# Kernel tuning notes

Hardware: AMD Instinct MI355X
Metric: run time of the kernel (lower is better)

Reference implementation:

```python
import jax, jax.numpy as jnp
import numpy as np

EPS = 1e-6


def _layernorm(x, g, b):
    mu = jnp.mean(x, axis=-1, keepdims=True)
    var = jnp.mean((x - mu) ** 2, axis=-1, keepdims=True)
    return (x - mu) * jax.lax.rsqrt(var + EPS) * g + b


def _sinusoidal_pe(seq_len, d_model):
    pos = jnp.arange(seq_len, dtype=jnp.float32)[:, None]
    div = jnp.exp(jnp.arange(0, d_model, 2, dtype=jnp.float32) * (-np.log(10000.0) / d_model))
    pe = jnp.zeros((seq_len, d_model), dtype=jnp.float32)
    pe = pe.at[:, 0::2].set(jnp.sin(pos * div))
    pe = pe.at[:, 1::2].set(jnp.cos(pos * div))
    return pe


def setup_inputs() -> dict:
    key = jax.random.key(0)
    ks = jax.random.split(key, 6)
    B, S, D, H = 4, 4096, 1024, 16
    std = 0.02
    return {
        "x": jax.random.normal(ks[0], (B, S, D), jnp.float32),
        "ln1_g": jnp.ones((D,), jnp.float32),
        "ln1_b": jnp.zeros((D,), jnp.float32),
        "w_qkv": jax.random.normal(ks[1], (D, 3 * D), jnp.float32) * std,
        "w_out": jax.random.normal(ks[2], (D, D), jnp.float32) * std,
        "b_out": jnp.zeros((D,), jnp.float32),
        "ln2_g": jnp.ones((D,), jnp.float32),
        "ln2_b": jnp.zeros((D,), jnp.float32),
        "w1": jax.random.normal(ks[3], (D, 2 * D), jnp.float32) * std,
        "b1": jnp.zeros((2 * D,), jnp.float32),
        "w2": jax.random.normal(ks[4], (2 * D, 2 * D), jnp.float32) * std,
        "b2": jnp.zeros((2 * D,), jnp.float32),
        "w3": jax.random.normal(ks[5], (2 * D, D), jnp.float32) * std,
        "b3": jnp.zeros((D,), jnp.float32),
    }


def reference(x, ln1_g, ln1_b, w_qkv, w_out, b_out, ln2_g, ln2_b, w1, b1, w2, b2, w3, b3):
    B, S, D = x.shape
    H = 16
    dh = D // H  # dim_head = 64

    h = _layernorm(x, ln1_g, ln1_b)
    h = h + _sinusoidal_pe(S, D)[None]  # space_dim == 1 -> sinusoidal PE

    # linear (kernelized, non-causal) self-attention: efficient-attention style
    qkv = h @ w_qkv  # [B,S,3D]
    q, k, v = jnp.split(qkv, 3, axis=-1)
    to_heads = lambda t: t.reshape(B, S, H, dh).transpose(0, 2, 1, 3)  # [B,H,S,dh]
    q, k, v = to_heads(q), to_heads(k), to_heads(v)
    q = jax.nn.softmax(q, axis=-1) * (dh ** -0.5)
    k = jax.nn.softmax(k, axis=2)  # softmax over sequence
    context = jnp.einsum('bhnd,bhne->bhde', k, v)  # [B,H,dh,dh]
    attn = jnp.einsum('bhnd,bhde->bhne', q, context)  # [B,H,S,dh]
    attn = attn.transpose(0, 2, 1, 3).reshape(B, S, D)
    attn = attn @ w_out + b_out

    x = x + attn  # residual (dropout p=0)

    y = _layernorm(x, ln2_g, ln2_b)
    y = jax.nn.gelu(y @ w1 + b1, approximate=False)
    y = jax.nn.gelu(y @ w2 + b2, approximate=False)
    y = y @ w3 + b3
    return x + y
```

## Files before the change

kernel.cpp:

```cpp
#include <hip/hip_runtime.h>
#include <cstdint>
#include <cstddef>

#define BB 4
#define SS 4096
#define DD 1024
#define HH 16
#define MM (BB*SS)

typedef __bf16 bf16x8 __attribute__((ext_vector_type(8)));
typedef float  f32x4  __attribute__((ext_vector_type(4)));

__device__ __forceinline__ float b2f(unsigned short h){
    union { unsigned int u; float f; } c; c.u = ((unsigned int)h) << 16; return c.f;
}
__device__ __forceinline__ unsigned short f2b(float f){
    union { float f; unsigned int u; } c; c.f = f;
    unsigned int u = c.u + 0x7FFFu + ((c.u >> 16) & 1u);
    return (unsigned short)(u >> 16);
}

__global__ void transpose_cvt(const float* __restrict__ src, unsigned short* __restrict__ dst,
                              int K, int N){
    __shared__ float tile[32][33];
    int kb = blockIdx.y*32, nb = blockIdx.x*32;
    int tx = threadIdx.x, ty = threadIdx.y;
    for(int i=0;i<32;i+=8) tile[ty+i][tx] = src[(size_t)(kb+ty+i)*N + nb+tx];
    __syncthreads();
    for(int i=0;i<32;i+=8) dst[(size_t)(nb+ty+i)*K + kb+tx] = f2b(tile[tx][ty+i]);
}

__global__ __launch_bounds__(256) void ln_kernel(const float* __restrict__ x,
                                                 const float* __restrict__ g,
                                                 const float* __restrict__ bta,
                                                 unsigned short* __restrict__ out,
                                                 int add_pe){
    int row = blockIdx.x;
    int t = threadIdx.x;
    float4 v = ((const float4*)(x + (size_t)row*DD))[t];
    float s = v.x+v.y+v.z+v.w;
    float q = v.x*v.x+v.y*v.y+v.z*v.z+v.w*v.w;
    for(int off=32; off>0; off>>=1){ s += __shfl_xor(s, off); q += __shfl_xor(q, off); }
    __shared__ float red[8];
    int wv = t>>6, ln = t&63;
    if(ln==0){ red[wv] = s; red[4+wv] = q; }
    __syncthreads();
    s = red[0]+red[1]+red[2]+red[3];
    q = red[4]+red[5]+red[6]+red[7];
    float mu = s * (1.0f/1024.0f);
    float var = q * (1.0f/1024.0f) - mu*mu;
    float rs = rsqrtf(var + 1e-6f);
    int d0 = t*4;
    float4 gg = ((const float4*)g)[t];
    float4 bb = ((const float4*)bta)[t];
    float o0 = (v.x-mu)*rs*gg.x + bb.x;
    float o1 = (v.y-mu)*rs*gg.y + bb.y;
    float o2 = (v.z-mu)*rs*gg.z + bb.z;
    float o3 = (v.w-mu)*rs*gg.w + bb.w;
    if(add_pe){
        int sidx = row & (SS-1);
        const float cfac = -0.008994473019508968f;
        float a0 = (float)sidx * expf(cfac * (float)(d0));
        float a1 = (float)sidx * expf(cfac * (float)(d0 + 2));
        o0 += sinf(a0); o1 += cosf(a0);
        o2 += sinf(a1); o3 += cosf(a1);
    }
    ushort4 o;
    o.x = f2b(o0); o.y = f2b(o1); o.z = f2b(o2); o.w = f2b(o3);
    *(ushort4*)(out + (size_t)row*DD + d0) = o;
}

template<int EPI>
__global__ __launch_bounds__(256, 2) void gemm_bt(
        const unsigned short* __restrict__ A,
        const unsigned short* __restrict__ Bt,
        void* __restrict__ Cout,
        const float* __restrict__ bias,
        const float* __restrict__ resid,
        int M, int N, int K)
{
    __shared__ __align__(16) unsigned short lA[128*64];
    __shared__ __align__(16) unsigned short lB[128*64];
    const int tid  = threadIdx.x;
    const int lane = tid & 63;
    const int wave = tid >> 6;
    const int quad = lane >> 4;
    const int l16  = lane & 15;
    const int wr = wave >> 1, wc = wave & 1;

    int gn  = gridDim.x;
    int lin = blockIdx.y * gn + blockIdx.x;
    int xcd = lin & 7;
    int j   = lin >> 3;
    int mt  = xcd + 8*(j/gn);
    int nt  = j - (j/gn)*gn;
    const int m0 = mt * 128;
    const int n0 = nt * 128;

    f32x4 acc[4][4] = {};

    for (int k0 = 0; k0 < K; k0 += 64) {
        __syncthreads();
        #pragma unroll
        for (int i = 0; i < 4; i++) {
            int c   = tid + 256*i;
            int row = c >> 3;
            int kc  = ((c & 7) ^ (row & 7)) << 3;
            const unsigned short* gA = A  + (size_t)(m0 + row) * K + k0 + kc;
            const unsigned short* gB = Bt + (size_t)(n0 + row) * K + k0 + kc;
            char* lpA = ((char*)lA) + (wave<<10) + (i<<12);
            char* lpB = ((char*)lB) + (wave<<10) + (i<<12);
            __builtin_amdgcn_global_load_lds((const __attribute__((address_space(1))) void*)gA,
                                             (__attribute__((address_space(3))) void*)lpA, 16, 0, 0);
            __builtin_amdgcn_global_load_lds((const __attribute__((address_space(1))) void*)gB,
                                             (__attribute__((address_space(3))) void*)lpB, 16, 0, 0);
        }
        __syncthreads();
        #pragma unroll
        for (int kk = 0; kk < 2; kk++) {
            bf16x8 af[4], bfr[4];
            #pragma unroll
            for (int mi = 0; mi < 4; mi++) {
                int row = wr*64 + mi*16 + l16;
                int kb  = (kk*64 + quad*16) ^ ((row & 7) << 4);
                af[mi] = *(const bf16x8*)((const char*)lA + row*128 + kb);
            }
            #pragma unroll
            for (int ni = 0; ni < 4; ni++) {
                int row = wc*64 + ni*16 + l16;
                int kb  = (kk*64 + quad*16) ^ ((row & 7) << 4);
                bfr[ni] = *(const bf16x8*)((const char*)lB + row*128 + kb);
            }
            #pragma unroll
            for (int mi = 0; mi < 4; mi++)
                #pragma unroll
                for (int ni = 0; ni < 4; ni++)
                    acc[mi][ni] = __builtin_amdgcn_mfma_f32_16x16x32_bf16(af[mi], bfr[ni], acc[mi][ni], 0, 0, 0);
        }
    }

    #pragma unroll
    for (int mi = 0; mi < 4; mi++) {
        #pragma unroll
        for (int r = 0; r < 4; r++) {
            int grow = m0 + wr*64 + mi*16 + quad*4 + r;
            #pragma unroll
            for (int ni = 0; ni < 4; ni++) {
                int gcol = n0 + wc*64 + ni*16 + l16;
                float v = acc[mi][ni][r];
                size_t idx = (size_t)grow * N + gcol;
                if (EPI == 0) {
                    ((unsigned short*)Cout)[idx] = f2b(v);
                } else if (EPI == 1) {
                    v += bias[gcol];
                    v = 0.5f * v * (1.0f + erff(v * 0.70710678118654752f));
                    ((unsigned short*)Cout)[idx] = f2b(v);
                } else {
                    v += bias[gcol] + resid[idx];
                    ((float*)Cout)[idx] = v;
                }
            }
        }
    }
}

__global__ __launch_bounds__(256) void ctx_partial(const unsigned short* __restrict__ qkv,
                                                   float* __restrict__ EP,
                                                   float* __restrict__ CS){
    int sc = blockIdx.x, h = blockIdx.y, b = blockIdx.z;
    int t = threadIdx.x;
    __shared__ __align__(16) float kl[64][64];
    __shared__ __align__(16) float vl[64][64];
    __shared__ float csred[4][64];
    float acc[16] = {};
    float cspart = 0.0f;
    int e = t & 63, dg = (t >> 6) * 16;
    int dcol = t & 63, schunk = t >> 6;
    for(int s0 = 0; s0 < 256; s0 += 64){
        __syncthreads();
        for(int j=0;j<4;j++){
            int lin = t + 256*j;
            int row = lin >> 4;
            int c4  = (lin & 15) * 4;
            size_t gr = (size_t)(b*SS + sc*256 + s0 + row);
            ushort4 kv = *(const ushort4*)(qkv + gr*3072 + DD + h*64 + c4);
            float4 kf; kf.x=expf(b2f(kv.x)); kf.y=expf(b2f(kv.y)); kf.z=expf(b2f(kv.z)); kf.w=expf(b2f(kv.w));
            *(float4*)&kl[row][c4] = kf;
            ushort4 vv = *(const ushort4*)(qkv + gr*3072 + 2*DD + h*64 + c4);
            float4 vf; vf.x=b2f(vv.x); vf.y=b2f(vv.y); vf.z=b2f(vv.z); vf.w=b2f(vv.w);
            *(float4*)&vl[row][c4] = vf;
        }
        __syncthreads();
        #pragma unroll
        for(int i=0;i<16;i++) cspart += kl[schunk*16+i][dcol];
        for(int s=0;s<64;s++){
            float ve = vl[s][e];
            #pragma unroll
            for(int di=0; di<16; di++) acc[di] += kl[s][dg+di] * ve;
        }
    }
    int slot = (b*HH + h)*16 + sc;
    float* ep = EP + (size_t)slot*4096;
    #pragma unroll
    for(int di=0; di<16; di++) ep[(dg+di)*64 + e] = acc[di];
    csred[schunk][dcol] = cspart;
    __syncthreads();
    if(t < 64) CS[slot*64 + t] = csred[0][t]+csred[1][t]+csred[2][t]+csred[3][t];
}

__global__ __launch_bounds__(256) void ctx_reduce(const float* __restrict__ EP,
                                                  const float* __restrict__ CS,
                                                  float* __restrict__ CTXF){
    int bh = blockIdx.x;
    int t = threadIdx.x;
    int d = t >> 2, e0 = (t & 3) * 16;
    float cs = 0.0f;
    #pragma unroll
    for(int sl=0; sl<16; sl++) cs += CS[(bh*16+sl)*64 + d];
    float inv = 1.0f/cs;
    #pragma unroll
    for(int i=0;i<16;i++){
        float s = 0.0f;
        #pragma unroll
        for(int sl=0; sl<16; sl++) s += EP[(size_t)(bh*16+sl)*4096 + d*64 + e0 + i];
        CTXF[(size_t)bh*4096 + d*64 + e0 + i] = s * inv;
    }
}

__global__ __launch_bounds__(256) void attn_heads(const unsigned short* __restrict__ qkv,
                                                  const float* __restrict__ CTXF,
                                                  unsigned short* __restrict__ abuf){
    int rg = blockIdx.x, h = blockIdx.y;
    int b = rg >> 6;
    int t = threadIdx.x;
    __shared__ __align__(16) float cl[64][64];
    __shared__ float ql[64*65];
    const float* cb = CTXF + (size_t)(b*HH + h)*4096;
    for(int j=0;j<4;j++){
        int lin = t + 256*j;
        ((float4*)cl)[lin] = ((const float4*)cb)[lin];
    }
    {
        int r = t >> 2, seg = (t & 3) * 16;
        const unsigned short* qp = qkv + (size_t)(rg*64 + r)*3072 + h*64 + seg;
        float vals[16];
        float m = -1e30f;
        #pragma unroll
        for(int u=0; u<4; u++){
            ushort4 qv = *(const ushort4*)(qp + u*4);
            vals[u*4+0]=b2f(qv.x); vals[u*4+1]=b2f(qv.y); vals[u*4+2]=b2f(qv.z); vals[u*4+3]=b2f(qv.w);
        }
        #pragma unroll
        for(int i=0;i<16;i++) m = fmaxf(m, vals[i]);
        m = fmaxf(m, __shfl_xor(m, 1));
        m = fmaxf(m, __shfl_xor(m, 2));
        float ssum = 0.0f;
        #pragma unroll
        for(int i=0;i<16;i++){ vals[i] = expf(vals[i]-m); ssum += vals[i]; }
        ssum += __shfl_xor(ssum, 1);
        ssum += __shfl_xor(ssum, 2);
        float scl = 0.125f/ssum;
        #pragma unroll
        for(int i=0;i<16;i++) ql[r*65 + seg + i] = vals[i]*scl;
    }
    __syncthreads();
    int e = t & 63, rbase = (t >> 6) * 16;
    float acc2[16] = {};
    for(int d=0; d<64; d++){
        float cv = cl[d][e];
        #pragma unroll
        for(int ri=0; ri<16; ri++) acc2[ri] += ql[(rbase+ri)*65 + d] * cv;
    }
    #pragma unroll
    for(int ri=0; ri<16; ri++)
        abuf[(size_t)(rg*64 + rbase + ri)*DD + h*64 + e] = f2b(acc2[ri]);
}

extern "C" void kernel_launch(void* const* d_in, const int* in_sizes, int n_in,
                              void* d_out, int out_size, void* d_ws, size_t ws_size,
                              hipStream_t stream)
{
    const float* x     = (const float*)d_in[0];
    const float* ln1_g = (const float*)d_in[1];
    const float* ln1_b = (const float*)d_in[2];
    const float* w_qkv = (const float*)d_in[3];
    const float* w_out = (const float*)d_in[4];
    const float* b_out = (const float*)d_in[5];
    const float* ln2_g = (const float*)d_in[6];
    const float* ln2_b = (const float*)d_in[7];
    const float* w1    = (const float*)d_in[8];
    const float* b1    = (const float*)d_in[9];
    const float* w2    = (const float*)d_in[10];
    const float* b2    = (const float*)d_in[11];
    const float* w3    = (const float*)d_in[12];
    const float* b3    = (const float*)d_in[13];

    char* ws = (char*)d_ws;
    unsigned short* wqkvT = (unsigned short*)(ws + 0);
    unsigned short* woutT = (unsigned short*)(ws + 6291456);
    unsigned short* w1T   = (unsigned short*)(ws + 8388608);
    unsigned short* w2T   = (unsigned short*)(ws + 12582912);
    unsigned short* w3T   = (unsigned short*)(ws + 20971520);
    unsigned short* Hbuf  = (unsigned short*)(ws + 25165824);
    unsigned short* QKV   = (unsigned short*)(ws + 58720256);
    float*          EP    = (float*)(ws + 159383552);
    float*          CS    = (float*)(ws + 176160768);
    float*          CTXF  = (float*)(ws + 176422912);
    unsigned short* Abuf  = Hbuf;
    float*          X2    = (float*)(ws + 58720256);
    unsigned short* H2    = Hbuf;
    unsigned short* Y1    = (unsigned short*)d_out;
    unsigned short* Y2    = (unsigned short*)(ws + 125829120);

    dim3 tb(32, 8);
    transpose_cvt<<<dim3(3072/32, 1024/32), tb, 0, stream>>>(w_qkv, wqkvT, 1024, 3072);
    transpose_cvt<<<dim3(1024/32, 1024/32), tb, 0, stream>>>(w_out, woutT, 1024, 1024);
    transpose_cvt<<<dim3(2048/32, 1024/32), tb, 0, stream>>>(w1,    w1T,   1024, 2048);
    transpose_cvt<<<dim3(2048/32, 2048/32), tb, 0, stream>>>(w2,    w2T,   2048, 2048);
    transpose_cvt<<<dim3(1024/32, 2048/32), tb, 0, stream>>>(w3,    w3T,   2048, 1024);

    ln_kernel<<<MM, 256, 0, stream>>>(x, ln1_g, ln1_b, Hbuf, 1);

    gemm_bt<0><<<dim3(3072/128, MM/128), 256, 0, stream>>>(Hbuf, wqkvT, QKV, nullptr, nullptr, MM, 3072, 1024);

    ctx_partial<<<dim3(16, HH, BB), 256, 0, stream>>>(QKV, EP, CS);
    ctx_reduce<<<BB*HH, 256, 0, stream>>>(EP, CS, CTXF);
    attn_heads<<<dim3(256, HH), 256, 0, stream>>>(QKV, CTXF, Abuf);

    gemm_bt<2><<<dim3(1024/128, MM/128), 256, 0, stream>>>(Abuf, woutT, X2, b_out, x, MM, 1024, 1024);

    ln_kernel<<<MM, 256, 0, stream>>>(X2, ln2_g, ln2_b, H2, 0);

    gemm_bt<1><<<dim3(2048/128, MM/128), 256, 0, stream>>>(H2, w1T, Y1, b1, nullptr, MM, 2048, 1024);
    gemm_bt<1><<<dim3(2048/128, MM/128), 256, 0, stream>>>(Y1, w2T, Y2, b2, nullptr, MM, 2048, 2048);
    gemm_bt<2><<<dim3(1024/128, MM/128), 256, 0, stream>>>(Y2, w3T, d_out, b3, X2, MM, 1024, 2048);
}
```

Baseline: 791.7 us.

## Store residual stream in bf16 and register-tile context/attention kernels

The intermediate residual X2 is now written as bf16 instead of fp32, and the second layernorm and final GEMM epilogue read it as bf16. This halves that tensor's write and read traffic but adds rounding error to the residual carried into the output. Separately, ctx_partial and attn_heads switch to 4x4 register tiles with float4 LDS reads, 16-byte global loads and vectorised stores, and a transposed q buffer in LDS, to cut LDS traffic per FMA.

```diff
diff --git a/kernel.cpp b/kernel.cpp
--- a/kernel.cpp
+++ b/kernel.cpp
@@ -13,6 +13,9 @@
 
 __device__ __forceinline__ float b2f(unsigned short h){
     union { unsigned int u; float f; } c; c.u = ((unsigned int)h) << 16; return c.f;
+}
+__device__ __forceinline__ float b2f_u(unsigned int u16){
+    union { unsigned int u; float f; } c; c.u = u16 << 16; return c.f;
 }
 __device__ __forceinline__ unsigned short f2b(float f){
     union { float f; unsigned int u; } c; c.f = f;
@@ -30,14 +33,21 @@
     for(int i=0;i<32;i+=8) dst[(size_t)(nb+ty+i)*K + kb+tx] = f2b(tile[tx][ty+i]);
 }
 
-__global__ __launch_bounds__(256) void ln_kernel(const float* __restrict__ x,
+template<int INBF>
+__global__ __launch_bounds__(256) void ln_kernel(const void* __restrict__ xin,
                                                  const float* __restrict__ g,
                                                  const float* __restrict__ bta,
                                                  unsigned short* __restrict__ out,
                                                  int add_pe){
     int row = blockIdx.x;
     int t = threadIdx.x;
-    float4 v = ((const float4*)(x + (size_t)row*DD))[t];
+    float4 v;
+    if (INBF == 0) {
+        v = ((const float4*)((const float*)xin + (size_t)row*DD))[t];
+    } else {
+        ushort4 u = ((const ushort4*)((const unsigned short*)xin + (size_t)row*DD))[t];
+        v.x = b2f(u.x); v.y = b2f(u.y); v.z = b2f(u.z); v.w = b2f(u.w);
+    }
     float s = v.x+v.y+v.z+v.w;
     float q = v.x*v.x+v.y*v.y+v.z*v.z+v.w*v.w;
     for(int off=32; off>0; off>>=1){ s += __shfl_xor(s, off); q += __shfl_xor(q, off); }
@@ -76,7 +86,7 @@
         const unsigned short* __restrict__ Bt,
         void* __restrict__ Cout,
         const float* __restrict__ bias,
-        const float* __restrict__ resid,
+        const void* __restrict__ resid,
         int M, int N, int K)
 {
     __shared__ __align__(16) unsigned short lA[128*64];
@@ -155,8 +165,11 @@
                     v += bias[gcol];
                     v = 0.5f * v * (1.0f + erff(v * 0.70710678118654752f));
                     ((unsigned short*)Cout)[idx] = f2b(v);
+                } else if (EPI == 2) {
+                    v += bias[gcol] + ((const float*)resid)[idx];
+                    ((unsigned short*)Cout)[idx] = f2b(v);
                 } else {
-                    v += bias[gcol] + resid[idx];
+                    v += bias[gcol] + b2f(((const unsigned short*)resid)[idx]);
                     ((float*)Cout)[idx] = v;
                 }
             }
@@ -172,37 +185,52 @@
     __shared__ __align__(16) float kl[64][64];
     __shared__ __align__(16) float vl[64][64];
     __shared__ float csred[4][64];
-    float acc[16] = {};
+    float acc[4][4] = {};
     float cspart = 0.0f;
-    int e = t & 63, dg = (t >> 6) * 16;
+    int e4 = (t & 15) * 4, d4 = (t >> 4) * 4;
     int dcol = t & 63, schunk = t >> 6;
     for(int s0 = 0; s0 < 256; s0 += 64){
         __syncthreads();
-        for(int j=0;j<4;j++){
+        #pragma unroll
+        for(int j=0;j<2;j++){
             int lin = t + 256*j;
-            int row = lin >> 4;
-            int c4  = (lin & 15) * 4;
+            int row = lin >> 3;
+            int c8  = (lin & 7) * 8;
             size_t gr = (size_t)(b*SS + sc*256 + s0 + row);
-            ushort4 kv = *(const ushort4*)(qkv + gr*3072 + DD + h*64 + c4);
-            float4 kf; kf.x=expf(b2f(kv.x)); kf.y=expf(b2f(kv.y)); kf.z=expf(b2f(kv.z)); kf.w=expf(b2f(kv.w));
-            *(float4*)&kl[row][c4] = kf;
-            ushort4 vv = *(const ushort4*)(qkv + gr*3072 + 2*DD + h*64 + c4);
-            float4 vf; vf.x=b2f(vv.x); vf.y=b2f(vv.y); vf.z=b2f(vv.z); vf.w=b2f(vv.w);
-            *(float4*)&vl[row][c4] = vf;
+            uint4 kv = *(const uint4*)(qkv + gr*3072 + DD + h*64 + c8);
+            float4 ka, kb2;
+            ka.x = expf(b2f_u(kv.x & 0xFFFFu)); ka.y = expf(b2f_u(kv.x >> 16));
+            ka.z = expf(b2f_u(kv.y & 0xFFFFu)); ka.w = expf(b2f_u(kv.y >> 16));
+            kb2.x = expf(b2f_u(kv.z & 0xFFFFu)); kb2.y = expf(b2f_u(kv.z >> 16));
+            kb2.z = expf(b2f_u(kv.w & 0xFFFFu)); kb2.w = expf(b2f_u(kv.w >> 16));
+            *(float4*)&kl[row][c8]   = ka;
+            *(float4*)&kl[row][c8+4] = kb2;
+            uint4 vv = *(const uint4*)(qkv + gr*3072 + 2*DD + h*64 + c8);
+            float4 va, vb;
+            va.x = b2f_u(vv.x & 0xFFFFu); va.y = b2f_u(vv.x >> 16);
+            va.z = b2f_u(vv.y & 0xFFFFu); va.w = b2f_u(vv.y >> 16);
+            vb.x = b2f_u(vv.z & 0xFFFFu); vb.y = b2f_u(vv.z >> 16);
+            vb.z = b2f_u(vv.w & 0xFFFFu); vb.w = b2f_u(vv.w >> 16);
+            *(float4*)&vl[row][c8]   = va;
+            *(float4*)&vl[row][c8+4] = vb;
         }
         __syncthreads();
         #pragma unroll
         for(int i=0;i<16;i++) cspart += kl[schunk*16+i][dcol];
         for(int s=0;s<64;s++){
-            float ve = vl[s][e];
-            #pragma unroll
-            for(int di=0; di<16; di++) acc[di] += kl[s][dg+di] * ve;
+            float4 k4 = *(const float4*)&kl[s][d4];
+            float4 v4 = *(const float4*)&vl[s][e4];
+            acc[0][0] += k4.x*v4.x; acc[0][1] += k4.x*v4.y; acc[0][2] += k4.x*v4.z; acc[0][3] += k4.x*v4.w;
+            acc[1][0] += k4.y*v4.x; acc[1][1] += k4.y*v4.y; acc[1][2] += k4.y*v4.z; acc[1][3] += k4.y*v4.w;
+            acc[2][0] += k4.z*v4.x; acc[2][1] += k4.z*v4.y; acc[2][2] += k4.z*v4.z; acc[2][3] += k4.z*v4.w;
+            acc[3][0] += k4.w*v4.x; acc[3][1] += k4.w*v4.y; acc[3][2] += k4.w*v4.z; acc[3][3] += k4.w*v4.w;
         }
     }
     int slot = (b*HH + h)*16 + sc;
     float* ep = EP + (size_t)slot*4096;
     #pragma unroll
-    for(int di=0; di<16; di++) ep[(dg+di)*64 + e] = acc[di];
+    for(int i=0;i<4;i++)
+        *(float4*)&ep[(d4+i)*64 + e4] = *(float4*)&acc[i][0];
     csred[schunk][dcol] = cspart;
     __syncthreads();
     if(t < 64) CS[slot*64 + t] = csred[0][t]+csred[1][t]+csred[2][t]+csred[3][t];
@@ -234,7 +262,7 @@
     int b = rg >> 6;
     int t = threadIdx.x;
     __shared__ __align__(16) float cl[64][64];
-    __shared__ float ql[64*65];
+    __shared__ __align__(16) float qlT[64*68];
     const float* cb = CTXF + (size_t)(b*HH + h)*4096;
     for(int j=0;j<4;j++){
         int lin = t + 256*j;
@@ -261,19 +289,25 @@
         ssum += __shfl_xor(ssum, 2);
         float scl = 0.125f/ssum;
         #pragma unroll
-        for(int i=0;i<16;i++) ql[r*65 + seg + i] = vals[i]*scl;
+        for(int i=0;i<16;i++) qlT[(seg+i)*68 + r] = vals[i]*scl;
     }
     __syncthreads();
-    int e = t & 63, rbase = (t >> 6) * 16;
-    float acc2[16] = {};
+    int e4 = (t & 15) * 4, r4 = (t >> 4) * 4;
+    float acc[4][4] = {};
     for(int d=0; d<64; d++){
-        float cv = cl[d][e];
-        #pragma unroll
-        for(int ri=0; ri<16; ri++) acc2[ri] += ql[(rbase+ri)*65 + d] * cv;
-    }
-    #pragma unroll
-    for(int ri=0; ri<16; ri++)
-        abuf[(size_t)(rg*64 + rbase + ri)*DD + h*64 + e] = f2b(acc2[ri]);
+        float4 q4 = *(const float4*)&qlT[d*68 + r4];
+        float4 c4 = *(const float4*)&cl[d][e4];
+        acc[0][0] += q4.x*c4.x; acc[0][1] += q4.x*c4.y; acc[0][2] += q4.x*c4.z; acc[0][3] += q4.x*c4.w;
+        acc[1][0] += q4.y*c4.x; acc[1][1] += q4.y*c4.y; acc[1][2] += q4.y*c4.z; acc[1][3] += q4.y*c4.w;
+        acc[2][0] += q4.z*c4.x; acc[2][1] += q4.z*c4.y; acc[2][2] += q4.z*c4.z; acc[2][3] += q4.z*c4.w;
+        acc[3][0] += q4.w*c4.x; acc[3][1] += q4.w*c4.y; acc[3][2] += q4.w*c4.z; acc[3][3] += q4.w*c4.w;
+    }
+    #pragma unroll
+    for(int i=0;i<4;i++){
+        ushort4 o;
+        o.x = f2b(acc[i][0]); o.y = f2b(acc[i][1]); o.z = f2b(acc[i][2]); o.w = f2b(acc[i][3]);
+        *(ushort4*)(abuf + (size_t)(rg*64 + r4 + i)*DD + h*64 + e4) = o;
+    }
 }
 
 extern "C" void kernel_launch(void* const* d_in, const int* in_sizes, int n_in,
@@ -307,7 +341,7 @@
     float*          CS    = (float*)(ws + 176160768);
     float*          CTXF  = (float*)(ws + 176422912);
     unsigned short* Abuf  = Hbuf;
-    float*          X2    = (float*)(ws + 58720256);
+    unsigned short* X2    = (unsigned short*)(ws + 58720256);
     unsigned short* H2    = Hbuf;
     unsigned short* Y1    = (unsigned short*)d_out;
     unsigned short* Y2    = (unsigned short*)(ws + 125829120);
@@ -319,7 +353,7 @@
     transpose_cvt<<<dim3(2048/32, 2048/32), tb, 0, stream>>>(w2,    w2T,   2048, 2048);
     transpose_cvt<<<dim3(1024/32, 2048/32), tb, 0, stream>>>(w3,    w3T,   2048, 1024);
 
-    ln_kernel<<<MM, 256, 0, stream>>>(x, ln1_g, ln1_b, Hbuf, 1);
+    ln_kernel<0><<<MM, 256, 0, stream>>>(x, ln1_g, ln1_b, Hbuf, 1);
 
     gemm_bt<0><<<dim3(3072/128, MM/128), 256, 0, stream>>>(Hbuf, wqkvT, QKV, nullptr, nullptr, MM, 3072, 1024);
 
@@ -329,9 +363,9 @@
 
     gemm_bt<2><<<dim3(1024/128, MM/128), 256, 0, stream>>>(Abuf, woutT, X2, b_out, x, MM, 1024, 1024);
 
-    ln_kernel<<<MM, 256, 0, stream>>>(X2, ln2_g, ln2_b, H2, 0);
+    ln_kernel<1><<<MM, 256, 0, stream>>>(X2, ln2_g, ln2_b, H2, 0);
 
     gemm_bt<1><<<dim3(2048/128, MM/128), 256, 0, stream>>>(H2, w1T, Y1, b1, nullptr, MM, 2048, 1024);
     gemm_bt<1><<<dim3(2048/128, MM/128), 256, 0, stream>>>(Y1, w2T, Y2, b2, nullptr, MM, 2048, 2048);
-    gemm_bt<2><<<dim3(1024/128, MM/128), 256, 0, stream>>>(Y2, w3T, d_out, b3, X2, MM, 1024, 2048);
-}
+    gemm_bt<3><<<dim3(1024/128, MM/128), 256, 0, stream>>>(Y2, w3T, d_out, b3, X2, MM, 1024, 2048);
+}
```

After: 730.6 us. 7.7% less time.
